# Kernel tuning notes

Hardware: AMD Instinct MI355X
Metric: run time of the kernel (lower is better)

Reference implementation:

```python
import jax, jax.numpy as jnp
import numpy as np

B, KLEN, QLEN = 16, 4096, 1
D_MODEL, HEADS, KERNELS = 1024, 8, 10
DIM = D_MODEL // HEADS  # 128
SCALE = 0.02


def setup_inputs() -> dict:
    key = jax.random.key(0)
    ks = jax.random.split(key, 12)
    return {
        "query": jax.random.normal(ks[0], (B, QLEN, D_MODEL), jnp.float32),
        "key_in": jax.random.normal(ks[1], (B, KLEN, D_MODEL), jnp.float32),
        "value": jax.random.normal(ks[2], (B, KLEN, D_MODEL), jnp.float32),
        "prev_align": jax.random.uniform(ks[3], (B, HEADS, KLEN), jnp.float32),
        # learned params
        "conv_w": jax.random.normal(ks[4], (KERNELS, HEADS, 3), jnp.float32) * SCALE,   # OIH, k=3
        "conv_b": jnp.zeros((KERNELS,), jnp.float32),
        "w_u": jax.random.normal(ks[5], (KERNELS, DIM), jnp.float32) * SCALE,
        "w_q": jax.random.normal(ks[6], (D_MODEL, HEADS * DIM), jnp.float32) * SCALE,
        "w_v": jax.random.normal(ks[7], (D_MODEL, HEADS * DIM), jnp.float32) * SCALE,
        "bias": jax.random.uniform(ks[8], (DIM,), jnp.float32, minval=-0.1, maxval=0.1),
        "score_w": jax.random.normal(ks[9], (DIM,), jnp.float32) * SCALE,
        "score_b": jnp.zeros((), jnp.float32),
    }


def reference(query, key_in, value, prev_align, conv_w, conv_b, w_u, w_q, w_v, bias, score_w, score_b):
    b, k_len = key_in.shape[0], key_in.shape[1]
    # location features: conv1d over k_len with heads as channels -> [B, KERNELS, k_len]
    loc = jax.lax.conv_general_dilated(
        prev_align, conv_w, window_strides=(1,), padding=[(1, 1)],
        dimension_numbers=("NCH", "OIH", "NCH")) + conv_b[None, :, None]
    loc_energy = jnp.tanh(jnp.einsum("bck,cd->bkd", loc, w_u))  # [B, k_len, DIM]
    # projections split into heads
    q = jnp.einsum("bqf,fe->bqe", query, w_q).reshape(b, QLEN, HEADS, DIM).transpose(0, 2, 1, 3)   # [B,H,1,DIM]
    k = jnp.einsum("bkf,fe->bke", key_in, w_v).reshape(b, k_len, HEADS, DIM).transpose(0, 2, 1, 3)  # [B,H,K,DIM]
    v = value.reshape(b, k_len, HEADS, DIM).transpose(0, 2, 1, 3)                                   # [B,H,K,DIM]
    # additive energy (q_len==1 broadcasts over keys)
    e = jnp.tanh(k + q + loc_energy[:, None] + bias)            # [B,H,K,DIM]
    score = jnp.einsum("bhkd,d->bhk", e, score_w) + score_b    # [B,H,K]
    align = jax.nn.softmax(score, axis=-1)
    context = jnp.einsum("bhk,bhkd->bhd", align, v).reshape(b * HEADS, DIM)
    return context, align
```

## Files before the change

kernel.cpp:

```cpp
#include <hip/hip_runtime.h>
#include <hip/hip_bf16.h>
#include <cstdint>

typedef __attribute__((ext_vector_type(8))) short bf16x8;
typedef __attribute__((ext_vector_type(4))) float f32x4;
typedef __attribute__((ext_vector_type(8))) unsigned short u16x8;
typedef __attribute__((ext_vector_type(4))) unsigned int u32x4;

__device__ __forceinline__ unsigned short f2bf(float f) {
    unsigned int u = __float_as_uint(f);
    unsigned int r = (u + 0x7fffu + ((u >> 16) & 1u)) >> 16;
    return (unsigned short)r;
}

__device__ __forceinline__ float tanh_fast(float x) {
    return 1.0f - 2.0f / (__expf(2.0f * x) + 1.0f);
}

#define GLDS(SRC, DST) __builtin_amdgcn_global_load_lds(                         \
        (const __attribute__((address_space(1))) void*)(SRC),                    \
        (__attribute__((address_space(3))) void*)(DST), 16, 0, 0)

__global__ __launch_bounds__(256) void prep_kernel(
        const float* __restrict__ wv, unsigned short* __restrict__ wvT,
        const float* __restrict__ query, const float* __restrict__ w_q,
        float* __restrict__ ws_q,
        const float* __restrict__ pa, const float* __restrict__ conv_w,
        const float* __restrict__ conv_b, const float* __restrict__ w_u,
        float* __restrict__ le) {
    __shared__ __align__(16) char smem[16640];
    const int bid = blockIdx.x;
    const int t = threadIdx.x;

    if (bid < 256) {
        float (*tile)[129] = reinterpret_cast<float(*)[129]>(smem);
        const int h = bid >> 5, kt = bid & 31;
        for (int i = t; i < 1024; i += 256) {
            const int fl = i >> 5;
            const int e4 = (i & 31) * 4;
            const float4 v = *reinterpret_cast<const float4*>(
                wv + (size_t)(kt * 32 + fl) * 1024 + h * 128 + e4);
            tile[fl][e4 + 0] = v.x; tile[fl][e4 + 1] = v.y;
            tile[fl][e4 + 2] = v.z; tile[fl][e4 + 3] = v.w;
        }
        __syncthreads();
#pragma unroll
        for (int cc2 = 0; cc2 < 2; ++cc2) {
            const int c = cc2 * 256 + t;
            const int cb = c >> 6, kg = (c >> 4) & 3, ccl = c & 15;
            const int e_local = cb * 16 + ccl;
            u16x8 u;
#pragma unroll
            for (int jj = 0; jj < 8; ++jj) u[jj] = f2bf(tile[kg * 8 + jj][e_local]);
            *reinterpret_cast<u16x8*>(wvT + (((size_t)h * 32 + kt) * 512 + c) * 8) = u;
        }
    } else if (bid < 384) {
        float* qs = reinterpret_cast<float*>(smem);
        const int bh = bid - 256;
        const int b = bh >> 3, h = bh & 7;
        for (int i = t; i < 1024; i += 256) qs[i] = query[(size_t)b * 1024 + i];
        __syncthreads();
        if (t < 128) {
            float acc = 0.f;
            const float* wcol = w_q + h * 128 + t;
            for (int f = 0; f < 1024; ++f) acc = fmaf(qs[f], wcol[(size_t)f * 1024], acc);
            ws_q[(size_t)bh * 128 + t] = acc;
        }
    } else {
        float* pas = reinterpret_cast<float*>(smem);
        float* wu_s = pas + 1056;
        float* cw = wu_s + 1280;
        float* cb = cw + 240;
        const int idx = bid - 384;
        const int b = idx >> 5, k0 = (idx & 31) * 128;
        for (int i = t; i < 8 * 130; i += 256) {
            const int hh = i / 130, kk = i % 130;
            const int gk = k0 + kk - 1;
            pas[hh * 132 + kk] = (gk >= 0 && gk < 4096)
                ? pa[((size_t)(b * 8 + hh)) * 4096 + gk] : 0.f;
        }
        for (int i = t; i < 1280; i += 256) wu_s[i] = w_u[i];
        if (t < 240) cw[t] = conv_w[t];
        if (t < 10) cb[t] = conv_b[t];
        __syncthreads();
        const int k = t >> 1;
        const int d0 = (t & 1) * 64;
        float lc[10];
#pragma unroll
        for (int c = 0; c < 10; ++c) {
            float acc = cb[c];
#pragma unroll
            for (int hh = 0; hh < 8; ++hh) {
                acc += pas[hh * 132 + k] * cw[(c * 8 + hh) * 3 + 0]
                     + pas[hh * 132 + k + 1] * cw[(c * 8 + hh) * 3 + 1]
                     + pas[hh * 132 + k + 2] * cw[(c * 8 + hh) * 3 + 2];
            }
            lc[c] = acc;
        }
        float* dst = le + ((size_t)(b * 4096) + k0 + k) * 128 + d0;
#pragma unroll
        for (int dd = 0; dd < 64; dd += 4) {
            float4 o;
#pragma unroll
            for (int jj = 0; jj < 4; ++jj) {
                float s = 0.f;
#pragma unroll
                for (int c = 0; c < 10; ++c) s += lc[c] * wu_s[c * 128 + d0 + dd + jj];
                ((float*)&o)[jj] = tanh_fast(s);
            }
            *reinterpret_cast<float4*>(dst + dd) = o;
        }
    }
}

#define NT 32
__global__ __launch_bounds__(512) void gemm_score_kernel(
        const float* __restrict__ key_in, const unsigned short* __restrict__ wvT_tiled,
        const float* __restrict__ le,
        const float* __restrict__ ws_q, const float* __restrict__ bias,
        const float* __restrict__ score_w, const float* __restrict__ score_b,
        float* __restrict__ align_out) {
    __shared__ __align__(16) unsigned short As[3][4096];
    __shared__ __align__(16) unsigned short Bs[3][8192];
    __shared__ float qb_sm[256], sw_sm[128];
    __shared__ float partial[128][4];

    const int t = threadIdx.x;
    const int lane = t & 63, wid = t >> 6;
    const int wm = wid >> 2;
    const int wn = wid & 3;

    const int fid = blockIdx.x;
    const int x = fid & 7, j = fid >> 3;
    const int bm = x * 64 + (j >> 2);
    const int hp = j & 3;
    const int b = bm >> 5;
    const int kk0 = (bm & 31) << 7;

    if (t < 256) {
        const int hh = t >> 7, d = t & 127;
        qb_sm[t] = ws_q[(size_t)(b * 8 + hp * 2 + hh) * 128 + d] + bias[d];
        if (t < 128) sw_sm[t] = score_w[t];
    }

    const int r_ = t >> 2, ks = t & 3;
    const float* aRow = key_in + ((size_t)(b * 4096 + kk0) + r_) * 1024 + ks * 8;
    const int cW = (t >> 6) * 64 + ks * 16 + (r_ & 15);
    const int dst0 = (cW ^ (ks | ((ks & 1) << 2))) * 8;

    const int kgR = lane >> 4;
    const int laneSwz = lane ^ (kgR | ((kgR & 1) << 2));

    const unsigned short* bT = wvT_tiled
        + (size_t)(hp * 2 + (t >> 8)) * 131072 + (t & 255) * 8;
    const int dstB = (t >> 8) * 4096 + (t & 255) * 8;

    float4 st0, st1;

#define LOADA(KT) {                                                               \
        const float* p_ = aRow + (KT) * 32;                                       \
        st0 = *reinterpret_cast<const float4*>(p_);                               \
        st1 = *reinterpret_cast<const float4*>(p_ + 4); }

#define WRITEA(BUF) {                                                             \
        __hip_bfloat162 h0_ = __float22bfloat162_rn({st0.x, st0.y});              \
        __hip_bfloat162 h1_ = __float22bfloat162_rn({st0.z, st0.w});              \
        __hip_bfloat162 h2_ = __float22bfloat162_rn({st1.x, st1.y});              \
        __hip_bfloat162 h3_ = __float22bfloat162_rn({st1.z, st1.w});              \
        u32x4 u_;                                                                 \
        u_[0] = *reinterpret_cast<unsigned int*>(&h0_);                           \
        u_[1] = *reinterpret_cast<unsigned int*>(&h1_);                           \
        u_[2] = *reinterpret_cast<unsigned int*>(&h2_);                           \
        u_[3] = *reinterpret_cast<unsigned int*>(&h3_);                           \
        *reinterpret_cast<u32x4*>(&As[BUF][dst0]) = u_; }

#define STAGE_B(BUF, KT) {                                                        \
        GLDS(bT + (size_t)(KT) * 4096, &Bs[BUF][dstB]);                           \
        GLDS(bT + (size_t)(KT) * 4096 + 2048, &Bs[BUF][dstB + 2048]); }

    f32x4 acc[4][4] = {};

    LOADA(0);
    STAGE_B(0, 0);
    STAGE_B(1, 1);
    WRITEA(0);
    LOADA(1);

    for (int kt = 0; kt < NT; ++kt) {
        const int cur = kt % 3;
        const int nxt = (kt + 1) % 3;
        const int pre = (kt + 2) % 3;
        WRITEA(nxt);
        LOADA((kt + 2) & (NT - 1));
        asm volatile("s_waitcnt lgkmcnt(0)\n\t"
                     "s_barrier" ::: "memory");
        STAGE_B(pre, (kt + 2) & (NT - 1));

        bf16x8 af[4], bg[4];
#pragma unroll
        for (int mf = 0; mf < 4; ++mf)
            af[mf] = *reinterpret_cast<const bf16x8*>(
                &As[cur][((wm * 4 + mf) * 64 + laneSwz) * 8]);
#pragma unroll
        for (int nf = 0; nf < 4; ++nf)
            bg[nf] = *reinterpret_cast<const bf16x8*>(
                &Bs[cur][(wn >> 1) * 4096 + ((wn & 1) * 4 + nf) * 512 + lane * 8]);
        __builtin_amdgcn_s_setprio(1);
#pragma unroll
        for (int mf = 0; mf < 4; ++mf)
#pragma unroll
            for (int nf = 0; nf < 4; ++nf)
                acc[mf][nf] = __builtin_amdgcn_mfma_f32_16x16x32_bf16(
                    af[mf], bg[nf], acc[mf][nf], 0, 0, 0);
        __builtin_amdgcn_s_setprio(0);
    }

    const float K2 = 2.8853900817779268f;
    const float sb = score_b[0];
    const int g = lane >> 4;
    const int l15 = lane & 15;
    float kqb[4], swv[4];
#pragma unroll
    for (int nf = 0; nf < 4; ++nf) {
        const int d128 = (wn & 1) * 64 + nf * 16 + l15;
        kqb[nf] = qb_sm[(wn >> 1) * 128 + d128] * K2;
        swv[nf] = sw_sm[d128];
    }
    const float* leB = le + ((size_t)(b * 4096 + kk0) + wm * 64 + g * 4) * 128
                       + (wn & 1) * 64 + l15;

#pragma unroll
    for (int mf = 0; mf < 4; ++mf) {
        float lv[16];
#pragma unroll
        for (int jj = 0; jj < 4; ++jj)
#pragma unroll
            for (int nf = 0; nf < 4; ++nf)
                lv[jj * 4 + nf] = leB[(size_t)(mf * 16 + jj) * 128 + nf * 16];
#pragma unroll
        for (int jj = 0; jj < 4; ++jj) {
            const int row_l = wm * 64 + mf * 16 + g * 4 + jj;
            float sum = 0.f;
#pragma unroll
            for (int nf = 0; nf < 4; ++nf) {
                const float m = fmaf(K2, lv[jj * 4 + nf], kqb[nf]);
                const float tt = fmaf(K2, acc[mf][nf][jj], m);
                const float y = __builtin_amdgcn_exp2f(tt);
                const float r = fmaf(-2.0f, __builtin_amdgcn_rcpf(y + 1.0f), 1.0f);
                sum = fmaf(r, swv[nf], sum);
            }
            sum += __shfl_xor(sum, 1);
            sum += __shfl_xor(sum, 2);
            sum += __shfl_xor(sum, 4);
            sum += __shfl_xor(sum, 8);
            if (l15 == 0) partial[row_l][wn] = sum;
        }
    }
    __syncthreads();
    if (t < 256) {
        const int r = t >> 1, hh = t & 1;
        const float sc = partial[r][hh * 2] + partial[r][hh * 2 + 1] + sb;
        align_out[(size_t)(b * 8 + hp * 2 + hh) * 4096 + kk0 + r] = sc;
    }
}

__global__ __launch_bounds__(256) void softmax_kernel(float* __restrict__ align_o) {
    const int bh = blockIdx.x;
    float* row = align_o + (size_t)bh * 4096;
    const int t = threadIdx.x;
    float v[16];
    float m = -1e30f;
#pragma unroll
    for (int i = 0; i < 16; ++i) {
        v[i] = row[i * 256 + t];
        m = fmaxf(m, v[i]);
    }
#pragma unroll
    for (int off = 32; off; off >>= 1) m = fmaxf(m, __shfl_xor(m, off));
    __shared__ float sm[4], ss[4];
    const int wid = t >> 6;
    if ((t & 63) == 0) sm[wid] = m;
    __syncthreads();
    m = fmaxf(fmaxf(sm[0], sm[1]), fmaxf(sm[2], sm[3]));
    float s = 0.f;
#pragma unroll
    for (int i = 0; i < 16; ++i) {
        v[i] = __expf(v[i] - m);
        s += v[i];
    }
#pragma unroll
    for (int off = 32; off; off >>= 1) s += __shfl_xor(s, off);
    if ((t & 63) == 0) ss[wid] = s;
    __syncthreads();
    s = ss[0] + ss[1] + ss[2] + ss[3];
    const float inv = 1.f / s;
#pragma unroll
    for (int i = 0; i < 16; ++i) row[i * 256 + t] = v[i] * inv;
}

__global__ __launch_bounds__(256) void ctx_partial_kernel(
        const float* __restrict__ value, const float* __restrict__ align_o,
        float* __restrict__ pctx) {
    const int s = blockIdx.x;
    const int bh = blockIdx.y;
    const int b = bh >> 3, h = bh & 7;
    const int t = threadIdx.x;
    const int d4 = (t & 31) * 4;
    const int kg = t >> 5;
    const float* arow = align_o + (size_t)bh * 4096 + s * 128;
    const float* vbase = value + ((size_t)(b * 4096 + s * 128)) * 1024 + h * 128 + d4;
    float4 acc = {0.f, 0.f, 0.f, 0.f};
    for (int i = 0; i < 16; ++i) {
        const int kk = i * 8 + kg;
        const float a = arow[kk];
        const float4 v = *reinterpret_cast<const float4*>(vbase + (size_t)kk * 1024);
        acc.x += a * v.x; acc.y += a * v.y; acc.z += a * v.z; acc.w += a * v.w;
    }
    __shared__ float sm2[8][128];
    *reinterpret_cast<float4*>(&sm2[kg][d4]) = acc;
    __syncthreads();
    if (t < 128) {
        float s0 = 0.f;
#pragma unroll
        for (int gg = 0; gg < 8; ++gg) s0 += sm2[gg][t];
        pctx[((size_t)bh * 32 + s) * 128 + t] = s0;
    }
}

__global__ __launch_bounds__(128) void ctx_reduce_kernel(
        const float* __restrict__ pctx, float* __restrict__ out) {
    const int bh = blockIdx.x;
    const int t = threadIdx.x;
    float acc = 0.f;
    for (int s2 = 0; s2 < 32; ++s2) acc += pctx[((size_t)bh * 32 + s2) * 128 + t];
    out[(size_t)bh * 128 + t] = acc;
}

extern "C" void kernel_launch(void* const* d_in, const int* in_sizes, int n_in,
                              void* d_out, int out_size, void* d_ws, size_t ws_size,
                              hipStream_t stream) {
    const float* query   = (const float*)d_in[0];
    const float* key_in  = (const float*)d_in[1];
    const float* value   = (const float*)d_in[2];
    const float* pa      = (const float*)d_in[3];
    const float* conv_w  = (const float*)d_in[4];
    const float* conv_b  = (const float*)d_in[5];
    const float* w_u     = (const float*)d_in[6];
    const float* w_q     = (const float*)d_in[7];
    const float* w_v     = (const float*)d_in[8];
    const float* bias    = (const float*)d_in[9];
    const float* score_w = (const float*)d_in[10];
    const float* score_b = (const float*)d_in[11];

    float* out = (float*)d_out;
    float* ctx_out = out;
    float* align_out = out + 16384;

    char* ws = (char*)d_ws;
    const size_t OFF_Q    = 0;
    const size_t OFF_WVT  = 65536;
    const size_t OFF_PCTX = OFF_WVT + 2097152;
    const size_t OFF_LE   = OFF_PCTX + 2097152;

    float* ws_q            = (float*)(ws + OFF_Q);
    unsigned short* ws_wvT = (unsigned short*)(ws + OFF_WVT);
    float* ws_pctx         = (float*)(ws + OFF_PCTX);
    float* ws_le           = (float*)(ws + OFF_LE);

    hipLaunchKernelGGL(prep_kernel, dim3(896), dim3(256), 0, stream,
                       w_v, ws_wvT, query, w_q, ws_q,
                       pa, conv_w, conv_b, w_u, ws_le);
    hipLaunchKernelGGL(gemm_score_kernel, dim3(2048), dim3(512), 0, stream,
                       key_in, ws_wvT, ws_le, ws_q, bias, score_w, score_b, align_out);
    hipLaunchKernelGGL(softmax_kernel, dim3(128), dim3(256), 0, stream, align_out);
    hipLaunchKernelGGL(ctx_partial_kernel, dim3(32, 128), dim3(256), 0, stream, value, align_out, ws_pctx);
    hipLaunchKernelGGL(ctx_reduce_kernel, dim3(128), dim3(128), 0, stream, ws_pctx, ctx_out);
}
```

Baseline: 297.8 us.

## Replace context reduce kernel with atomics and shorten B-tile prefetch distance

Context accumulation now uses atomicAdd straight into the output, which an extra block in the prep kernel zeroes first. This removes the separate reduce kernel launch and the partial-context workspace round trip. The GEMM's B-tile async prefetch is also shortened from two stages ahead to one, issued at the top of each iteration. That could expose more global-load latency in exchange for a simpler schedule, and the atomics make the summation order nondeterministic.

After: 286.9 us. 3.6% less time.

```diff
diff --git a/kernel.cpp b/kernel.cpp
--- a/kernel.cpp
+++ b/kernel.cpp
@@ -27,7 +27,7 @@
         float* __restrict__ ws_q,
         const float* __restrict__ pa, const float* __restrict__ conv_w,
         const float* __restrict__ conv_b, const float* __restrict__ w_u,
-        float* __restrict__ le) {
+        float* __restrict__ le, float* __restrict__ ctx_out) {
     __shared__ __align__(16) char smem[16640];
     const int bid = blockIdx.x;
     const int t = threadIdx.x;
@@ -66,7 +66,7 @@
             for (int f = 0; f < 1024; ++f) acc = fmaf(qs[f], wcol[(size_t)f * 1024], acc);
             ws_q[(size_t)bh * 128 + t] = acc;
         }
-    } else {
+    } else if (bid < 896) {
         float* pas = reinterpret_cast<float*>(smem);
         float* wu_s = pas + 1056;
         float* cw = wu_s + 1280;
@@ -110,6 +110,10 @@
             }
             *reinterpret_cast<float4*>(dst + dd) = o;
         }
+    } else {
+        float4 z = {0.f, 0.f, 0.f, 0.f};
+        for (int i = t; i < 4096; i += 256)
+            *reinterpret_cast<float4*>(ctx_out + (size_t)i * 4) = z;
     }
 }
 
@@ -182,19 +186,17 @@
 
     LOADA(0);
     STAGE_B(0, 0);
-    STAGE_B(1, 1);
     WRITEA(0);
     LOADA(1);
 
     for (int kt = 0; kt < NT; ++kt) {
         const int cur = kt % 3;
         const int nxt = (kt + 1) % 3;
-        const int pre = (kt + 2) % 3;
+        STAGE_B(nxt, (kt + 1) & (NT - 1));
         WRITEA(nxt);
         LOADA((kt + 2) & (NT - 1));
         asm volatile("s_waitcnt lgkmcnt(0)\n\t"
                      "s_barrier" ::: "memory");
-        STAGE_B(pre, (kt + 2) & (NT - 1));
 
         bf16x8 af[4], bg[4];
 #pragma unroll
@@ -300,7 +302,7 @@
 
 __global__ __launch_bounds__(256) void ctx_partial_kernel(
         const float* __restrict__ value, const float* __restrict__ align_o,
-        float* __restrict__ pctx) {
+        float* __restrict__ ctx_out) {
     const int s = blockIdx.x;
     const int bh = blockIdx.y;
     const int b = bh >> 3, h = bh & 7;
@@ -323,17 +325,8 @@
         float s0 = 0.f;
 #pragma unroll
         for (int gg = 0; gg < 8; ++gg) s0 += sm2[gg][t];
-        pctx[((size_t)bh * 32 + s) * 128 + t] = s0;
-    }
-}
-
-__global__ __launch_bounds__(128) void ctx_reduce_kernel(
-        const float* __restrict__ pctx, float* __restrict__ out) {
-    const int bh = blockIdx.x;
-    const int t = threadIdx.x;
-    float acc = 0.f;
-    for (int s2 = 0; s2 < 32; ++s2) acc += pctx[((size_t)bh * 32 + s2) * 128 + t];
-    out[(size_t)bh * 128 + t] = acc;
+        atomicAdd(&ctx_out[(size_t)bh * 128 + t], s0);
+    }
 }
 
 extern "C" void kernel_launch(void* const* d_in, const int* in_sizes, int n_in,
@@ -359,20 +352,18 @@
     char* ws = (char*)d_ws;
     const size_t OFF_Q    = 0;
     const size_t OFF_WVT  = 65536;
-    const size_t OFF_PCTX = OFF_WVT + 2097152;
-    const size_t OFF_LE   = OFF_PCTX + 2097152;
+    const size_t OFF_LE   = OFF_WVT + 2097152;
 
     float* ws_q            = (float*)(ws + OFF_Q);
     unsigned short* ws_wvT = (unsigned short*)(ws + OFF_WVT);
-    float* ws_pctx         = (float*)(ws + OFF_PCTX);
     float* ws_le           = (float*)(ws + OFF_LE);
 
-    hipLaunchKernelGGL(prep_kernel, dim3(896), dim3(256), 0, stream,
+    hipLaunchKernelGGL(prep_kernel, dim3(897), dim3(256), 0, stream,
                        w_v, ws_wvT, query, w_q, ws_q,
-                       pa, conv_w, conv_b, w_u, ws_le);
+                       pa, conv_w, conv_b, w_u, ws_le, ctx_out);
     hipLaunchKernelGGL(gemm_score_kernel, dim3(2048), dim3(512), 0, stream,
                        key_in, ws_wvT, ws_le, ws_q, bias, score_w, score_b, align_out);
     hipLaunchKernelGGL(softmax_kernel, dim3(128), dim3(256), 0, stream, align_out);
-    hipLaunchKernelGGL(ctx_partial_kernel, dim3(32, 128), dim3(256), 0, stream, value, align_out, ws_pctx);
-    hipLaunchKernelGGL(ctx_reduce_kernel, dim3(128), dim3(128), 0, stream, ws_pctx, ctx_out);
-}
+    hipLaunchKernelGGL(ctx_partial_kernel, dim3(32, 128), dim3(256), 0, stream,
+                       value, align_out, ctx_out);
+}
```
